# Optimization experiments

Measured on AMD Instinct MI355X. Metric: run time of the kernel, lower is better.

## Reference

```python
import jax, jax.numpy as jnp
import numpy as np

B, T, ADIM = 64, 2048, 384
NUM_EMB, HID_DIM = 10, 3


def setup_inputs() -> dict:
    key = jax.random.key(0)
    ks = jax.random.split(key, 9)
    return {
        "hs_ref_embs": jax.random.normal(ks[0], (B, T, ADIM), dtype=jnp.float32),
        "inds": jax.random.randint(ks[1], (B, T), 0, NUM_EMB, dtype=jnp.int64),
        "codebook": jax.random.normal(ks[2], (NUM_EMB, HID_DIM), dtype=jnp.float32),
        "W_ih": jax.random.normal(ks[3], (4 * NUM_EMB, ADIM), dtype=jnp.float32) * 0.05,
        "W_hh": jax.random.normal(ks[4], (4 * NUM_EMB, NUM_EMB), dtype=jnp.float32) * 0.05,
        "b_ih": jax.random.normal(ks[5], (4 * NUM_EMB,), dtype=jnp.float32) * 0.05,
        "b_hh": jax.random.normal(ks[6], (4 * NUM_EMB,), dtype=jnp.float32) * 0.05,
        "qs_W": jax.random.normal(ks[7], (ADIM, HID_DIM), dtype=jnp.float32) * 0.05,
        "qs_b": jax.random.normal(ks[8], (ADIM,), dtype=jnp.float32) * 0.05,
    }


def _lstm_cell(x, h, c, W_ih, W_hh, b_ih, b_hh):
    # PyTorch LSTMCell: gates = x @ W_ih^T + b_ih + h @ W_hh^T + b_hh
    gates = x @ W_ih.T + b_ih + h @ W_hh.T + b_hh  # (B, 4H)
    i, f, g, o = jnp.split(gates, 4, axis=-1)
    i, f, o = jax.nn.sigmoid(i), jax.nn.sigmoid(f), jax.nn.sigmoid(o)
    g = jnp.tanh(g)
    c_new = f * c + i * g
    h_new = o * jnp.tanh(c_new)
    return h_new, c_new


def reference(hs_ref_embs, inds, codebook, W_ih, W_hh, b_ih, b_hh, qs_W, qs_b):
    Bsz, Tmax, _ = hs_ref_embs.shape
    H = codebook.shape[0]  # num_embeddings (= LSTM hidden size)
    D = codebook.shape[1]  # hidden_dim

    def step(carry, xs):
        h, c, prev_emb = carry
        x_t, is_first = xs
        qs = prev_emb @ qs_W.T + qs_b  # (B, adim)
        inp = jnp.where(is_first, x_t, x_t + qs)
        h, c = _lstm_cell(inp, h, c, W_ih, W_hh, b_ih, b_hh)
        scores = jax.nn.log_softmax(h, axis=-1)  # (B, H)
        top_ind = jnp.argmax(scores, axis=-1)    # top-1, indices not differentiated
        emb = codebook[top_ind]                  # (B, D) gather == one-hot matmul
        return (h, c, emb), (scores, emb)

    init = (
        jnp.zeros((Bsz, H), hs_ref_embs.dtype),
        jnp.zeros((Bsz, H), hs_ref_embs.dtype),
        jnp.zeros((Bsz, D), hs_ref_embs.dtype),
    )
    xs = (jnp.swapaxes(hs_ref_embs, 0, 1), jnp.arange(Tmax) == 0)
    _, (scores, embs) = jax.lax.scan(step, init, xs)
    scores = jnp.swapaxes(scores, 0, 1)  # (B, T, H) log-probs
    embs = jnp.swapaxes(embs, 0, 1)      # (B, T, D)
    # NLLLoss(mean): -mean over (B,T) of log-prob at ground-truth index
    picked = jnp.take_along_axis(scores, inds[..., None], axis=-1)[..., 0]
    loss = -jnp.mean(picked)
    return embs, loss
```

## Files before the change

kernel.cpp:

```cpp
#include <hip/hip_runtime.h>
#include <math.h>

#define BB 64
#define TT 2048
#define ADIM 384
#define NE 10
#define NG 40
#define HD 3

#define OFF_X32   0ULL
#define OFF_H     (41943040ULL + 126400ULL)
#define OFF_IDX   (OFF_H + 5242880ULL)
#define OFF_PART  (OFF_IDX + 524288ULL)
#define OFF_DUMP  (OFF_PART + 4096ULL)

__device__ __forceinline__ float fexp2(float x) {
    float r;
    asm("v_exp_f32 %0, %1" : "=v"(r) : "v"(x));
    return r;
}
__device__ __forceinline__ float frcp(float d) {
    float r;
    asm("v_rcp_f32 %0, %1" : "=v"(r) : "v"(d));
    return r;
}

template<int CTRL>
__device__ __forceinline__ float dpp_mov_f32(float x) {
    int v = __float_as_int(x);
    v = __builtin_amdgcn_update_dpp(v, v, CTRL, 0xF, 0xF, true);
    return __int_as_float(v);
}
template<int CTRL, int RMASK>
__device__ __forceinline__ unsigned dpp_mov_u32(unsigned x) {
    int v = __builtin_amdgcn_update_dpp((int)x, (int)x, CTRL, RMASK, 0xF, true);
    return (unsigned)v;
}
__device__ __forceinline__ unsigned umax2(unsigned a, unsigned b) {
    return a > b ? a : b;
}

__global__ __launch_bounds__(256) void gemm_kernel(
        const float* __restrict__ hs, const float* __restrict__ W_ih,
        float* __restrict__ X32) {
    int lane = threadIdx.x & 63;
    int wv = threadIdx.x >> 6;
    int cb = __builtin_amdgcn_readfirstlane(wv * 10);
    long row = (long)blockIdx.x * 64 + lane;
    const float* xr = hs + row * ADIM;
    float accA[10], accB[10];
#pragma unroll
    for (int j = 0; j < 10; ++j) { accA[j] = 0.0f; accB[j] = 0.0f; }
    for (int a0 = 0; a0 < ADIM; a0 += 4) {
        float4 xv = *(const float4*)(xr + a0);
#pragma unroll
        for (int j = 0; j < 10; ++j) {
            float4 wv4 = *(const float4*)(W_ih + (cb + j) * ADIM + a0);
            accA[j] = fmaf(wv4.x, xv.x, accA[j]);
            accA[j] = fmaf(wv4.y, xv.y, accA[j]);
            accB[j] = fmaf(wv4.z, xv.z, accB[j]);
            accB[j] = fmaf(wv4.w, xv.w, accB[j]);
        }
    }
    float* op = X32 + row * NG + cb;
#pragma unroll
    for (int j = 0; j < 10; ++j) op[j] = accA[j] + accB[j];
}

__global__ __launch_bounds__(256) void recur_tail_kernel(
        const float* __restrict__ W_ih, const float* __restrict__ codebook,
        const float* __restrict__ qs_W, const float* __restrict__ qs_b,
        const float* __restrict__ b_ih, const float* __restrict__ b_hh,
        const float* __restrict__ W_hh, const int* __restrict__ inds,
        float* __restrict__ out_embs, char* __restrict__ ws) {
    __shared__ double red[256];
    const int b = blockIdx.x;
    const int tid = threadIdx.x;

    if (tid < 64) {
        const int k = tid;
        const int j = k & 3;
        const int m = k >> 2;
        const bool valid = (k < NG);
        const int col = valid ? (j * 10 + m) : (NG - 1);
        const bool isg = (j == 2);

        double M0 = 0, M1 = 0, M2 = 0, qbd = 0;
        for (int a = 0; a < ADIM; ++a) {
            double w = (double)W_ih[col * ADIM + a];
            M0 = fma(w, (double)qs_W[a * HD + 0], M0);
            M1 = fma(w, (double)qs_W[a * HD + 1], M1);
            M2 = fma(w, (double)qs_W[a * HD + 2], M2);
            qbd = fma(w, (double)qs_b[a], qbd);
        }
        double biasd = (double)b_ih[col] + (double)b_hh[col];
        float etab[NE];
#pragma unroll
        for (int i = 0; i < NE; ++i) {
            double e = biasd + qbd;
            e = fma((double)codebook[i * HD + 0], M0, e);
            e = fma((double)codebook[i * HD + 1], M1, e);
            e = fma((double)codebook[i * HD + 2], M2, e);
            etab[i] = (float)e;
        }
        float esel = (float)biasd;

        const float LOG2E = 1.44269504088896340736f;
        const float Lg   = isg ? (-2.0f * LOG2E) : (-LOG2E);
        const float amul = isg ? 2.0f : 1.0f;
        const float aadd = isg ? -1.0f : 0.0f;
        const float L2   = -2.0f * LOG2E;

        float whh[NE];
#pragma unroll
        for (int mm = 0; mm < NE; ++mm) whh[mm] = W_hh[col * NE + mm];

        const float* Xb = (const float*)(ws + OFF_X32) + (long)b * TT * NG;

        const bool is_h = ((k & 3) == 0) && valid;
        const bool is_i = (k == NG);
        unsigned voff = is_h ? (unsigned)(OFF_H + ((unsigned)b * TT * NE + m) * 4u)
                      : is_i ? (unsigned)(OFF_IDX + (unsigned)b * TT * 4u)
                             : (unsigned)(OFF_DUMP + (unsigned)b * 256u);
        const unsigned vstep = is_h ? (unsigned)(NE * 4) : is_i ? 4u : 0u;
        const unsigned vmask = valid ? 0xFFFFFFFFu : 0u;

        float xs0 = Xb[0 * NG + col];
        float xs1 = Xb[1 * NG + col];
        float xs2 = Xb[2 * NG + col];
        float xs3 = Xb[3 * NG + col];

        float ha[NE];
#pragma unroll
        for (int mm = 0; mm < NE; ++mm) ha[mm] = 0.0f;
        float c = 0.0f;

        auto step = [&](float& xslot, int t) {
            float xg = xslot;
            xslot = Xb[(t + 4) * NG + col];

            float p0 = fmaf(ha[1], whh[1], ha[0] * whh[0]);
            float p1 = fmaf(ha[3], whh[3], ha[2] * whh[2]);
            float p2 = fmaf(ha[5], whh[5], ha[4] * whh[4]);
            float p3 = fmaf(ha[7], whh[7], ha[6] * whh[6]);
            float p4 = fmaf(ha[9], whh[9], ha[8] * whh[8]);
            float dotE = ((p0 + p1) + (p2 + p3)) + (p4 + esel);
            float g32 = xg + dotE;

            float e1 = fexp2(g32 * Lg);
            float r1 = frcp(1.0f + e1);
            float act = fmaf(amul, r1, aadd);

            float fiv = dpp_mov_f32<0x00>(act);
            float ffv = dpp_mov_f32<0x55>(act);
            float fgv = dpp_mov_f32<0xAA>(act);
            float fov = dpp_mov_f32<0xFF>(act);
            c = fmaf(ffv, c, fiv * fgv);

            float e2 = fexp2(fabsf(c) * L2);
            float r2 = frcp(1.0f + e2);
            float th = fmaf(2.0f, r2, -1.0f);
            float habs = fov * th;
            int hI = __float_as_int(habs) | (__float_as_int(c) & 0x80000000);

            int smsk = hI >> 31;
            unsigned key0 = ((unsigned)(hI ^ (smsk | (int)0x80000000))) & vmask;
            unsigned kr = umax2(key0, dpp_mov_u32<0x124, 0xF>(key0));
            kr = umax2(kr, dpp_mov_u32<0x128, 0xF>(kr));
            kr = umax2(kr, dpp_mov_u32<0x142, 0xA>(kr));
            kr = umax2(kr, dpp_mov_u32<0x143, 0xC>(kr));
            unsigned sMax = (unsigned)__builtin_amdgcn_readlane((int)kr, 32);
            unsigned long long ball = __ballot(key0 == sMax);
            int s_idx = ((int)__builtin_ctzll(ball)) >> 2;

            int val = is_h ? hI : s_idx;
            *(int*)(ws + voff) = val;
            voff += vstep;

#pragma unroll
            for (int mm = 0; mm < NE; ++mm)
                ha[mm] = __int_as_float(__builtin_amdgcn_readlane(hI, 4 * mm));

            float a0 = (s_idx & 1) ? etab[1] : etab[0];
            float a1 = (s_idx & 1) ? etab[3] : etab[2];
            float a2 = (s_idx & 1) ? etab[5] : etab[4];
            float a3 = (s_idx & 1) ? etab[7] : etab[6];
            float a4 = (s_idx & 1) ? etab[9] : etab[8];
            float b0 = (s_idx & 2) ? a1 : a0;
            float b1 = (s_idx & 2) ? a3 : a2;
            float c0 = (s_idx & 4) ? b1 : b0;
            esel = (s_idx & 8) ? a4 : c0;
        };

        for (int t = 0; t < TT; t += 4) {
            step(xs0, t);
            step(xs1, t + 1);
            step(xs2, t + 2);
            step(xs3, t + 3);
        }
    }

    __syncthreads();

    const float* h_ws = (const float*)(ws + OFF_H);
    const int* idx_ws = (const int*)(ws + OFF_IDX);
    double psum = 0.0;
    for (int t = tid; t < TT; t += 256) {
        long i = (long)b * TT + t;
        int idx = idx_ws[i];
        out_embs[i * 3 + 0] = codebook[idx * 3 + 0];
        out_embs[i * 3 + 1] = codebook[idx * 3 + 1];
        out_embs[i * 3 + 2] = codebook[idx * 3 + 2];

        const float* hp = h_ws + i * NE;
        double hv[NE];
#pragma unroll
        for (int mm = 0; mm < NE; ++mm) hv[mm] = (double)hp[mm];
        double mx = hv[0];
#pragma unroll
        for (int mm = 1; mm < NE; ++mm) mx = fmax(mx, hv[mm]);
        double sdn = 0.0;
#pragma unroll
        for (int mm = 0; mm < NE; ++mm) sdn += exp(hv[mm] - mx);
        int ind = inds[i];
        psum += (double)hp[ind] - (mx + log(sdn));
    }
    red[tid] = psum;
    __syncthreads();
    for (int st = 128; st > 0; st >>= 1) {
        if (tid < st) red[tid] += red[tid + st];
        __syncthreads();
    }
    if (tid == 0) ((double*)(ws + OFF_PART))[b] = red[0];
}

__global__ __launch_bounds__(64) void final_kernel(
        const double* __restrict__ partials, float* __restrict__ out_loss) {
    if (threadIdx.x == 0) {
        double s = 0.0;
        for (int i = 0; i < BB; ++i) s += partials[i];
        out_loss[0] = (float)(-s / (double)(BB * TT));
    }
}

extern "C" void kernel_launch(void* const* d_in, const int* in_sizes, int n_in,
                              void* d_out, int out_size, void* d_ws, size_t ws_size,
                              hipStream_t stream) {
    const float* hs       = (const float*)d_in[0];
    const int*   inds     = (const int*)d_in[1];
    const float* codebook = (const float*)d_in[2];
    const float* W_ih     = (const float*)d_in[3];
    const float* W_hh     = (const float*)d_in[4];
    const float* b_ih     = (const float*)d_in[5];
    const float* b_hh     = (const float*)d_in[6];
    const float* qs_W     = (const float*)d_in[7];
    const float* qs_b     = (const float*)d_in[8];
    float* out = (float*)d_out;

    char* ws = (char*)d_ws;
    float*  X32  = (float*)(ws + OFF_X32);
    double* part = (double*)(ws + OFF_PART);

    gemm_kernel<<<2048, 256, 0, stream>>>(hs, W_ih, X32);
    recur_tail_kernel<<<BB, 256, 0, stream>>>(W_ih, codebook, qs_W, qs_b,
                                              b_ih, b_hh, W_hh, inds, out, ws);
    final_kernel<<<1, 64, 0, stream>>>(part, out + (size_t)BB * TT * HD);
}
```

Baseline: 536.6 us.

## Fuse final loss reduction into tail kernel and simplify argmax key

Drops the separate final reduction kernel: each block adds its fixed-point partial loss into a global atomic accumulator, and the last block to arrive (tracked by an atomic counter) writes the loss. The counters are zeroed at the start of the GEMM kernel. The per-step argmax in the serial recurrence is also rewritten to pack the lane index into the low bits of the float key, so an fmax DPP reduction plus one readlane replaces the unsigned max, ballot and ctz. This removes a kernel launch and shortens the latency-bound recurrence step, at the cost of fixed-point rounding in the loss and argmax ties broken on perturbed low mantissa bits.

```diff
diff --git a/kernel.cpp b/kernel.cpp
--- a/kernel.cpp
+++ b/kernel.cpp
@@ -11,8 +11,11 @@
 #define OFF_X32   0ULL
 #define OFF_H     (41943040ULL + 126400ULL)
 #define OFF_IDX   (OFF_H + 5242880ULL)
-#define OFF_PART  (OFF_IDX + 524288ULL)
-#define OFF_DUMP  (OFF_PART + 4096ULL)
+#define OFF_ACC   (OFF_IDX + 524288ULL)
+#define OFF_CNT   (OFF_ACC + 8ULL)
+#define OFF_DUMP  (OFF_ACC + 4096ULL)
+
+#define FIXSCALE  1099511627776.0
 
 __device__ __forceinline__ float fexp2(float x) {
     float r;
@@ -32,17 +35,20 @@
     return __int_as_float(v);
 }
 template<int CTRL, int RMASK>
-__device__ __forceinline__ unsigned dpp_mov_u32(unsigned x) {
-    int v = __builtin_amdgcn_update_dpp((int)x, (int)x, CTRL, RMASK, 0xF, true);
-    return (unsigned)v;
-}
-__device__ __forceinline__ unsigned umax2(unsigned a, unsigned b) {
-    return a > b ? a : b;
+__device__ __forceinline__ float dpp_mov_f32m(float x) {
+    int v = __float_as_int(x);
+    v = __builtin_amdgcn_update_dpp(v, v, CTRL, RMASK, 0xF, true);
+    return __int_as_float(v);
 }
 
 __global__ __launch_bounds__(256) void gemm_kernel(
         const float* __restrict__ hs, const float* __restrict__ W_ih,
-        float* __restrict__ X32) {
+        char* __restrict__ ws) {
+    if (blockIdx.x == 0 && threadIdx.x == 0) {
+        *(unsigned long long*)(ws + OFF_ACC) = 0ull;
+        *(unsigned*)(ws + OFF_CNT) = 0u;
+    }
+    float* X32 = (float*)(ws + OFF_X32);
     int lane = threadIdx.x & 63;
     int wv = threadIdx.x >> 6;
     int cb = __builtin_amdgcn_readfirstlane(wv * 10);
@@ -121,9 +127,11 @@
         const bool is_i = (k == NG);
         unsigned voff = is_h ? (unsigned)(OFF_H + ((unsigned)b * TT * NE + m) * 4u)
                       : is_i ? (unsigned)(OFF_IDX + (unsigned)b * TT * 4u)
-                             : (unsigned)(OFF_DUMP + (unsigned)b * 256u);
+                             : (unsigned)(OFF_DUMP + (unsigned)b * 256u + (unsigned)k * 4u);
         const unsigned vstep = is_h ? (unsigned)(NE * 4) : is_i ? 4u : 0u;
-        const unsigned vmask = valid ? 0xFFFFFFFFu : 0u;
+
+        const unsigned kAnd = valid ? 0xFFFFFFF0u : 0u;
+        const unsigned kOr  = valid ? (unsigned)(15 - m) : 0xFF800000u;
 
         float xs0 = Xb[0 * NG + col];
         float xs1 = Xb[1 * NG + col];
@@ -160,18 +168,16 @@
             float e2 = fexp2(fabsf(c) * L2);
             float r2 = frcp(1.0f + e2);
             float th = fmaf(2.0f, r2, -1.0f);
-            float habs = fov * th;
-            int hI = __float_as_int(habs) | (__float_as_int(c) & 0x80000000);
-
-            int smsk = hI >> 31;
-            unsigned key0 = ((unsigned)(hI ^ (smsk | (int)0x80000000))) & vmask;
-            unsigned kr = umax2(key0, dpp_mov_u32<0x124, 0xF>(key0));
-            kr = umax2(kr, dpp_mov_u32<0x128, 0xF>(kr));
-            kr = umax2(kr, dpp_mov_u32<0x142, 0xA>(kr));
-            kr = umax2(kr, dpp_mov_u32<0x143, 0xC>(kr));
-            unsigned sMax = (unsigned)__builtin_amdgcn_readlane((int)kr, 32);
-            unsigned long long ball = __ballot(key0 == sMax);
-            int s_idx = ((int)__builtin_ctzll(ball)) >> 2;
+            float h = __builtin_copysignf(fov * th, c);
+            int hI = __float_as_int(h);
+
+            float key = __int_as_float((int)(((unsigned)hI & kAnd) | kOr));
+            key = fmaxf(key, dpp_mov_f32m<0x124, 0xF>(key));
+            key = fmaxf(key, dpp_mov_f32m<0x128, 0xF>(key));
+            key = fmaxf(key, dpp_mov_f32m<0x142, 0xA>(key));
+            key = fmaxf(key, dpp_mov_f32m<0x143, 0xC>(key));
+            int slo = __builtin_amdgcn_readlane(__float_as_int(key), 32);
+            int s_idx = 15 - (slo & 15);
 
             int val = is_h ? hI : s_idx;
             *(int*)(ws + voff) = val;
@@ -231,15 +237,21 @@
         if (tid < st) red[tid] += red[tid + st];
         __syncthreads();
     }
-    if (tid == 0) ((double*)(ws + OFF_PART))[b] = red[0];
-}
-
-__global__ __launch_bounds__(64) void final_kernel(
-        const double* __restrict__ partials, float* __restrict__ out_loss) {
-    if (threadIdx.x == 0) {
-        double s = 0.0;
-        for (int i = 0; i < BB; ++i) s += partials[i];
-        out_loss[0] = (float)(-s / (double)(BB * TT));
+    if (tid == 0) {
+        long long contrib = (long long)llrint(red[0] * FIXSCALE);
+        atomicAdd((unsigned long long*)(ws + OFF_ACC),
+                  (unsigned long long)contrib);
+        __threadfence();
+        unsigned old = atomicAdd((unsigned*)(ws + OFF_CNT), 1u);
+        if (old == BB - 1) {
+            __threadfence();
+            long long tot = (long long)__hip_atomic_load(
+                (unsigned long long*)(ws + OFF_ACC),
+                __ATOMIC_ACQUIRE, __HIP_MEMORY_SCOPE_AGENT);
+            double s = (double)tot * (1.0 / FIXSCALE);
+            out_embs[(size_t)BB * TT * HD] =
+                (float)(-s / (double)(BB * TT));
+        }
     }
 }
 
@@ -258,11 +270,8 @@
     float* out = (float*)d_out;
 
     char* ws = (char*)d_ws;
-    float*  X32  = (float*)(ws + OFF_X32);
-    double* part = (double*)(ws + OFF_PART);
-
-    gemm_kernel<<<2048, 256, 0, stream>>>(hs, W_ih, X32);
+
+    gemm_kernel<<<2048, 256, 0, stream>>>(hs, W_ih, ws);
     recur_tail_kernel<<<BB, 256, 0, stream>>>(W_ih, codebook, qs_W, qs_b,
                                               b_ih, b_hh, W_hh, inds, out, ws);
-    final_kernel<<<1, 64, 0, stream>>>(part, out + (size_t)BB * TT * HD);
-}
+}
```

After: 543.7 us. About the same (+1.3%).
